# Kernel optimization log

Measured on AMD Instinct MI355X. Metric: run time of the kernel, lower is better.

Reference implementation:

```python
import jax, jax.numpy as jnp
import numpy as np

N = 50000   # nodes
E = 800000  # edges
D = 128     # feature / hidden dim
G = 64      # graphs in batch
L = 3       # GCN layers
EPS = 1e-5  # LayerNorm eps (torch default)


def setup_inputs() -> dict:
    key = jax.random.key(0)
    ks = jax.random.split(key, 6)
    x = jax.random.normal(ks[0], (N, D), dtype=jnp.float32)
    edge_index = jax.random.randint(ks[1], (2, E), 0, N)
    batch = jnp.sort(jax.random.randint(ks[2], (N,), 0, G))
    Ws = jax.random.normal(ks[3], (L, D, D), dtype=jnp.float32) / np.sqrt(D).astype(np.float32)
    bs = jnp.zeros((L, D), dtype=jnp.float32)
    gammas = jnp.ones((L, D), dtype=jnp.float32)
    betas = jnp.zeros((L, D), dtype=jnp.float32)
    return {"x": x, "edge_index": edge_index, "batch": batch,
            "Ws": Ws, "bs": bs, "gammas": gammas, "betas": betas,
            "num_graphs": G}


def _layernorm(h, g, b):
    mu = jnp.mean(h, axis=-1, keepdims=True)
    var = jnp.mean((h - mu) ** 2, axis=-1, keepdims=True)
    return g * (h - mu) * jax.lax.rsqrt(var + EPS) + b


def reference(x, edge_index, batch, Ws, bs, gammas, betas, num_graphs):
    n = x.shape[0]
    loop = jnp.arange(n)
    # GCNConv adds self-loops; symmetric normalization on augmented graph
    src = jnp.concatenate([edge_index[0], loop])
    dst = jnp.concatenate([edge_index[1], loop])
    deg = jax.ops.segment_sum(jnp.ones_like(dst, dtype=x.dtype), dst, num_segments=n)
    dinv = jax.lax.rsqrt(jnp.maximum(deg, 1.0))  # deg >= 1 via self-loops
    norm_e = dinv[src] * dinv[dst]               # [E+N]

    h = x
    for i in range(Ws.shape[0]):
        hw = h @ Ws[i]                           # [N, D] dense GEMM
        msg = hw[src] * norm_e[:, None]          # gather + edge scale
        h = jax.ops.segment_sum(msg, dst, num_segments=n) + bs[i]  # scatter-add
        h = jax.nn.relu(_layernorm(h, gammas[i], betas[i]))
        # dropout is identity in eval mode

    # global mean pool over graph ids
    s = jax.ops.segment_sum(h, batch, num_segments=num_graphs)
    cnt = jax.ops.segment_sum(jnp.ones((n,), x.dtype), batch, num_segments=num_graphs)
    return s / jnp.maximum(cnt, 1.0)[:, None]
```

## Files before the change

### kernel.cpp

```cpp
#include <hip/hip_runtime.h>
#include <math.h>


#define NDIM 128
#define LN_EPS 1e-5f
#define NGRAPH 64
#define EPB 2048

typedef __attribute__((ext_vector_type(8))) short short8;
typedef __attribute__((ext_vector_type(8))) ushort ushort8;
typedef __attribute__((ext_vector_type(4))) float f32x4;

__device__ __forceinline__ ushort f2bf(float f) {
    unsigned u = __float_as_uint(f);
    return (ushort)((u + 0x7FFF + ((u >> 16) & 1)) >> 16);
}
__device__ __forceinline__ float bf2f(ushort b) {
    return __uint_as_float(((unsigned)b) << 16);
}

__device__ __forceinline__ uint block_excl_scan(uint v, uint* s) {
    int t = threadIdx.x;
    s[t] = v; __syncthreads();
    #pragma unroll
    for (int off = 1; off < 256; off <<= 1) {
        uint x = (t >= off) ? s[t - off] : 0u;
        __syncthreads();
        s[t] += x;
        __syncthreads();
    }
    uint incl = s[t];
    __syncthreads();
    return incl - v;
}


__global__ __launch_bounds__(256) void k_h1(const int* __restrict__ dst, uint* __restrict__ hist, int E) {
    __shared__ uint h[256];
    int t = threadIdx.x, b = blockIdx.x;
    h[t] = 0; __syncthreads();
    int e0 = b * EPB;
    #pragma unroll
    for (int i = 0; i < 8; i++) {
        int e = e0 + i * 256 + t;
        if (e < E) atomicAdd(&h[((uint)dst[e]) >> 8], 1u);
    }
    __syncthreads();
    hist[(size_t)b * 256 + t] = h[t];
}

__global__ __launch_bounds__(256) void k_colscan(uint* __restrict__ hist, uint* __restrict__ colsum, int EB) {
    __shared__ uint s[256];
    int t = threadIdx.x, j = blockIdx.x;
    uint v0 = (2 * t     < EB) ? hist[(size_t)(2 * t) * 256 + j] : 0u;
    uint v1 = (2 * t + 1 < EB) ? hist[(size_t)(2 * t + 1) * 256 + j] : 0u;
    uint pair = v0 + v1;
    uint excl = block_excl_scan(pair, s);
    if (2 * t < EB)     hist[(size_t)(2 * t) * 256 + j] = excl;
    if (2 * t + 1 < EB) hist[(size_t)(2 * t + 1) * 256 + j] = excl + v0;
    if (t == 255) colsum[j] = excl + pair;
}

__global__ __launch_bounds__(256) void k_scatter1(const int* __restrict__ src, const int* __restrict__ dst,
                                                  const uint* __restrict__ hist, const uint* __restrict__ colsum,
                                                  uint* __restrict__ ebuf, int E) {
    __shared__ uint s[256];
    __shared__ uint off[256];
    __shared__ uint cur[256];
    int t = threadIdx.x, b = blockIdx.x;
    uint er = block_excl_scan(colsum[t], s);
    off[t] = er + hist[(size_t)b * 256 + t];
    cur[t] = 0;
    __syncthreads();
    int e0 = b * EPB;
    #pragma unroll
    for (int i = 0; i < 8; i++) {
        int e = e0 + i * 256 + t;
        if (e < E) {
            uint d = (uint)dst[e], sv = (uint)src[e];
            uint bin = d >> 8;
            uint r = atomicAdd(&cur[bin], 1u);
            ebuf[off[bin] + r] = (d << 16) | sv;
        }
    }
}

__global__ __launch_bounds__(256) void k_sort2(const uint* __restrict__ ebuf, const uint* __restrict__ colsum,
                                               const int* __restrict__ batch,
                                               ushort* __restrict__ csr, int* __restrict__ base,
                                               int* __restrict__ deg, float* __restrict__ dinv,
                                               int* __restrict__ gstart, int* __restrict__ gend,
                                               const float* __restrict__ Ws, ushort* __restrict__ Wt,
                                               int N, int NB) {
    __shared__ uint h[256], nb[256], s[256], er_arr[256], ep_arr[256];
    int t = threadIdx.x, b = blockIdx.x;
    if (b >= NB) {
        int l = b - NB;
        const float* wsrc = Ws + (size_t)l * NDIM * NDIM;
        char* o = (char*)(Wt + (size_t)l * NDIM * NDIM);
        for (int idx = t; idx < NDIM * NDIM; idx += 256) {
            int k = idx >> 7, nn = idx & 127;
            int byte = ((nn * NDIM + k) * 2) ^ ((nn & 7) << 4);
            *(ushort*)(o + byte) = f2bf(wsrc[idx]);
        }
        return;
    }
    uint total = colsum[t];
    uint er = block_excl_scan(total, s);
    er_arr[t] = er;
    uint ep = block_excl_scan((total + 3u) & ~3u, s);
    ep_arr[t] = ep;
    __syncthreads();
    uint lo = er_arr[b];
    int cnt = (int)colsum[b];
    uint cb = ep_arr[b] + 768u * (uint)b;
    h[t] = 0; __syncthreads();
    for (int i = t; i < cnt; i += 256)
        atomicAdd(&h[(ebuf[lo + i] >> 16) & 255u], 1u);
    __syncthreads();
    uint dg = h[t];
    uint excl = block_excl_scan((dg + 3u) & ~3u, s);
    uint myb = cb + excl;
    nb[t] = myb;
    int n = b * 256 + t;
    if (n < N) {
        base[n] = (int)myb;
        deg[n] = (int)dg;
        dinv[n] = rsqrtf((float)(dg + 1u));
        int g = batch[n];
        if (n == 0 || batch[n - 1] != g) gstart[g] = n;
        if (n == N - 1 || batch[n + 1] != g) gend[g] = n + 1;
    }
    h[t] = 0; __syncthreads();
    for (int i = t; i < cnt; i += 256) {
        uint e = ebuf[lo + i];
        uint bin = (e >> 16) & 255u;
        uint r = atomicAdd(&h[bin], 1u);
        csr[nb[bin] + r] = (ushort)(e & 0xFFFFu);
    }
}


template <bool AF32>
__global__ __launch_bounds__(256) void k_gemm(const void* __restrict__ Ap, const ushort* __restrict__ Wt,
                                              ushort* __restrict__ C, const float* __restrict__ dinv, int N) {
    __shared__ char sW[32768];
    __shared__ ushort sC[64 * NDIM];
    int tid = threadIdx.x;
    {
        const float4* g = (const float4*)Wt;
        float4* s = (float4*)sW;
        #pragma unroll
        for (int i = 0; i < 8; i++) s[tid + 256 * i] = g[tid + 256 * i];
    }
    __syncthreads();

    int wave = tid >> 6, lane = tid & 63;
    int l15 = lane & 15, lhi = lane >> 4;
    int rw = blockIdx.x * 64 + wave * 16;

    f32x4 acc[8];
    #pragma unroll
    for (int n = 0; n < 8; n++) acc[n] = f32x4{0.f, 0.f, 0.f, 0.f};

    const float*  Af = (const float*)Ap;
    const ushort* Ab = (const ushort*)Ap;

    #pragma unroll
    for (int ks = 0; ks < 4; ks++) {
        int k = ks * 32 + lhi * 8;
        short8 a = short8{};
        int r = rw + l15;
        if (r < N) {
            if (AF32) {
                float4 v0 = *(const float4*)&Af[(size_t)r * NDIM + k];
                float4 v1 = *(const float4*)&Af[(size_t)r * NDIM + k + 4];
                short8 t;
                t[0] = (short)f2bf(v0.x); t[1] = (short)f2bf(v0.y);
                t[2] = (short)f2bf(v0.z); t[3] = (short)f2bf(v0.w);
                t[4] = (short)f2bf(v1.x); t[5] = (short)f2bf(v1.y);
                t[6] = (short)f2bf(v1.z); t[7] = (short)f2bf(v1.w);
                a = t;
            } else {
                a = *(const short8*)&Ab[(size_t)r * NDIM + k];
            }
        }
        #pragma unroll
        for (int n = 0; n < 8; n++) {
            int nn = n * 16 + l15;
            int byte = (nn * 256 + k * 2) ^ ((nn & 7) << 4);
            short8 b = *(const short8*)(sW + byte);
            acc[n] = __builtin_amdgcn_mfma_f32_16x16x32_bf16(a, b, acc[n], 0, 0, 0);
        }
    }

    #pragma unroll
    for (int r = 0; r < 4; r++) {
        int row = rw + lhi * 4 + r;
        float dn = (row < N) ? dinv[row] : 0.f;
        #pragma unroll
        for (int n = 0; n < 8; n++)
            sC[(wave * 16 + lhi * 4 + r) * NDIM + n * 16 + l15] = f2bf(acc[n][r] * dn);
    }
    __syncthreads();
    int row0 = blockIdx.x * 64;
    #pragma unroll
    for (int i = 0; i < 4; i++) {
        int flat = tid + i * 256;
        int row = flat >> 4, c8 = (flat & 15) * 8;
        int gr = row0 + row;
        if (gr < N)
            *(short8*)&C[(size_t)gr * NDIM + c8] = *(const short8*)&sC[row * NDIM + c8];
    }
}


__global__ __launch_bounds__(256) void k_agg(const ushort* __restrict__ hw, ushort* __restrict__ out,
                                             const float* __restrict__ dinv, const int* __restrict__ base,
                                             const int* __restrict__ deg, const ushort* __restrict__ csr,
                                             const float* __restrict__ bias, const float* __restrict__ gamma,
                                             const float* __restrict__ beta, int N) {
    int gtid = blockIdx.x * 256 + threadIdx.x;
    int n = gtid >> 5;
    int l4 = threadIdx.x & 31;
    if (n >= N) return;

    const ushort4* hv = (const ushort4*)hw;
    ushort4 sv = hv[(size_t)n * 32 + l4];
    float a0 = bf2f(sv.x), a1 = bf2f(sv.y), a2 = bf2f(sv.z), a3 = bf2f(sv.w);

    int b0 = base[n], dg = deg[n];
    int nfull = dg & ~7;
    ushort4 sa, sb;
    if (nfull > 0) {
        sa = *(const ushort4*)&csr[b0];
        sb = *(const ushort4*)&csr[b0 + 4];
    }
    for (int i = 0; i < nfull; i += 8) {
        ushort4 ca = sa, cb = sb;
        if (i + 8 < nfull) {
            sa = *(const ushort4*)&csr[b0 + i + 8];
            sb = *(const ushort4*)&csr[b0 + i + 12];
        }
        ushort4 t0 = hv[(size_t)ca.x * 32 + l4];
        ushort4 t1 = hv[(size_t)ca.y * 32 + l4];
        ushort4 t2 = hv[(size_t)ca.z * 32 + l4];
        ushort4 t3 = hv[(size_t)ca.w * 32 + l4];
        ushort4 t4 = hv[(size_t)cb.x * 32 + l4];
        ushort4 t5 = hv[(size_t)cb.y * 32 + l4];
        ushort4 t6 = hv[(size_t)cb.z * 32 + l4];
        ushort4 t7 = hv[(size_t)cb.w * 32 + l4];
        a0 += bf2f(t0.x) + bf2f(t1.x) + bf2f(t2.x) + bf2f(t3.x)
            + bf2f(t4.x) + bf2f(t5.x) + bf2f(t6.x) + bf2f(t7.x);
        a1 += bf2f(t0.y) + bf2f(t1.y) + bf2f(t2.y) + bf2f(t3.y)
            + bf2f(t4.y) + bf2f(t5.y) + bf2f(t6.y) + bf2f(t7.y);
        a2 += bf2f(t0.z) + bf2f(t1.z) + bf2f(t2.z) + bf2f(t3.z)
            + bf2f(t4.z) + bf2f(t5.z) + bf2f(t6.z) + bf2f(t7.z);
        a3 += bf2f(t0.w) + bf2f(t1.w) + bf2f(t2.w) + bf2f(t3.w)
            + bf2f(t4.w) + bf2f(t5.w) + bf2f(t6.w) + bf2f(t7.w);
    }
    for (int i = nfull; i < dg; i++) {
        int s = csr[b0 + i];
        ushort4 t = hv[(size_t)s * 32 + l4];
        a0 += bf2f(t.x); a1 += bf2f(t.y); a2 += bf2f(t.z); a3 += bf2f(t.w);
    }

    float dn = dinv[n];
    a0 *= dn; a1 *= dn; a2 *= dn; a3 *= dn;

    float4 bv = ((const float4*)bias)[l4];
    a0 += bv.x; a1 += bv.y; a2 += bv.z; a3 += bv.w;

    float s1 = a0 + a1 + a2 + a3;
    float s2 = a0 * a0 + a1 * a1 + a2 * a2 + a3 * a3;
    #pragma unroll
    for (int o = 1; o < 32; o <<= 1) {
        s1 += __shfl_xor(s1, o);
        s2 += __shfl_xor(s2, o);
    }
    float mu = s1 * (1.f / NDIM);
    float var = s2 * (1.f / NDIM) - mu * mu;
    float rs = rsqrtf(var + LN_EPS);

    float4 gv = ((const float4*)gamma)[l4];
    float4 be = ((const float4*)beta)[l4];
    ushort4 y;
    y.x = f2bf(fmaxf(gv.x * (a0 - mu) * rs + be.x, 0.f));
    y.y = f2bf(fmaxf(gv.y * (a1 - mu) * rs + be.y, 0.f));
    y.z = f2bf(fmaxf(gv.z * (a2 - mu) * rs + be.z, 0.f));
    y.w = f2bf(fmaxf(gv.w * (a3 - mu) * rs + be.w, 0.f));
    ((ushort4*)out)[(size_t)n * 32 + l4] = y;
}


__global__ __launch_bounds__(256) void k_pool2(const ushort* __restrict__ h, const int* __restrict__ gstart,
                                               const int* __restrict__ gend, float* __restrict__ out) {
    __shared__ float ps[16][128];
    int t = threadIdx.x, g = blockIdx.x;
    int st = gstart[g], en = gend[g];
    int rslot = t >> 4, dc = (t & 15) * 8;
    float acc[8] = {0.f, 0.f, 0.f, 0.f, 0.f, 0.f, 0.f, 0.f};
    for (int r = st + rslot; r < en; r += 16) {
        ushort8 v = *(const ushort8*)&h[(size_t)r * NDIM + dc];
        #pragma unroll
        for (int j = 0; j < 8; j++) acc[j] += bf2f(v[j]);
    }
    #pragma unroll
    for (int j = 0; j < 8; j++) ps[rslot][dc + j] = acc[j];
    __syncthreads();
    if (t < 128) {
        float s = 0.f;
        #pragma unroll
        for (int k = 0; k < 16; k++) s += ps[k][t];
        float c = (float)(en - st);
        out[g * NDIM + t] = s / fmaxf(c, 1.f);
    }
}


extern "C" void kernel_launch(void* const* d_in, const int* in_sizes, int n_in,
                              void* d_out, int out_size, void* d_ws, size_t ws_size,
                              hipStream_t stream) {
    const float* x      = (const float*)d_in[0];
    const int*   ei     = (const int*)d_in[1];
    const int*   batch  = (const int*)d_in[2];
    const float* Ws     = (const float*)d_in[3];
    const float* bs     = (const float*)d_in[4];
    const float* gammas = (const float*)d_in[5];
    const float* betas  = (const float*)d_in[6];
    float* out = (float*)d_out;

    int N = in_sizes[0] / NDIM;
    int E = in_sizes[1] / 2;
    const int* src = ei;
    const int* dst = ei + E;
    int EB = (E + EPB - 1) / EPB;
    int NB = (N + 255) / 256;

    char* w = (char*)d_ws;
    auto alloc = [&](size_t bytes) { char* p = w; w += (bytes + 255) & ~(size_t)255; return p; };
    int*    deg    = (int*)alloc((size_t)N * 4);
    int*    base   = (int*)alloc((size_t)N * 4);
    float*  dinv   = (float*)alloc((size_t)N * 4);
    uint*   hist   = (uint*)alloc((size_t)EB * 256 * 4);
    uint*   colsum = (uint*)alloc(256 * 4);
    uint*   ebuf   = (uint*)alloc((size_t)E * 4);
    ushort* csr    = (ushort*)alloc(((size_t)E + 256u * 772u) * 2);
    int*    gse    = (int*)alloc(2 * NGRAPH * 4);
    int*    gstart = gse;
    int*    gend   = gse + NGRAPH;
    ushort* Wt     = (ushort*)alloc((size_t)3 * NDIM * NDIM * 2);
    ushort* bufA   = (ushort*)alloc((size_t)N * NDIM * 2);
    ushort* bufB   = (ushort*)alloc((size_t)N * NDIM * 2);

    k_h1<<<EB, 256, 0, stream>>>(dst, hist, E);
    k_colscan<<<256, 256, 0, stream>>>(hist, colsum, EB);
    k_scatter1<<<EB, 256, 0, stream>>>(src, dst, hist, colsum, ebuf, E);
    k_sort2<<<NB + 3, 256, 0, stream>>>(ebuf, colsum, batch, csr, base, deg, dinv,
                                        gstart, gend, Ws, Wt, N, NB);

    int gGemm = (N + 63) / 64;
    int gAgg  = (N * 32 + 255) / 256;
    for (int l = 0; l < 3; l++) {
        const ushort* wl = Wt + (size_t)l * NDIM * NDIM;
        if (l == 0)
            k_gemm<true><<<gGemm, 256, 0, stream>>>((const void*)x, wl, bufB, dinv, N);
        else
            k_gemm<false><<<gGemm, 256, 0, stream>>>((const void*)bufA, wl, bufB, dinv, N);
        k_agg<<<gAgg, 256, 0, stream>>>(bufB, bufA, dinv, base, deg, csr,
                                        bs + l * NDIM, gammas + l * NDIM, betas + l * NDIM, N);
    }

    k_pool2<<<NGRAPH, 256, 0, stream>>>(bufA, gstart, gend, out);
}
```

Measured before the change: 271.1 us.

## Fuse CSR build into two kernels using per-block bucketed arena

Merges the histogram, column-scan and scatter kernels into a single pass where each edge block locally sorts edges by destination bin into its own arena slice, recording per-bin offsets. The second-stage sort reads each block's chunk for its bin directly, using a fixed per-bin CSR capacity instead of a global prefix scan. Base and degree are packed into an int2 for a single load in aggregation. This removes two launches and a global scan, but the sort kernel now reads many small, scattered chunks serially per thread. It also relies on a fixed capacity of 8192 edges per 256-node bin, which could overflow on skewed graphs.

```diff
diff --git a/kernel.cpp b/kernel.cpp
--- a/kernel.cpp
+++ b/kernel.cpp
@@ -6,6 +6,7 @@
 #define LN_EPS 1e-5f
 #define NGRAPH 64
 #define EPB 2048
+#define CSR_CAP 8192
 
 typedef __attribute__((ext_vector_type(8))) short short8;
 typedef __attribute__((ext_vector_type(8))) ushort ushort8;
@@ -35,8 +36,9 @@
 }
 
 
-__global__ __launch_bounds__(256) void k_h1(const int* __restrict__ dst, uint* __restrict__ hist, int E) {
-    __shared__ uint h[256];
+__global__ __launch_bounds__(256) void k_build1(const int* __restrict__ src, const int* __restrict__ dst,
+                                                uint* __restrict__ hist, uint* __restrict__ arena, int E) {
+    __shared__ uint h[256], s[256], rank[256];
     int t = threadIdx.x, b = blockIdx.x;
     h[t] = 0; __syncthreads();
     int e0 = b * EPB;
@@ -46,53 +48,34 @@
         if (e < E) atomicAdd(&h[((uint)dst[e]) >> 8], 1u);
     }
     __syncthreads();
-    hist[(size_t)b * 256 + t] = h[t];
-}
-
-__global__ __launch_bounds__(256) void k_colscan(uint* __restrict__ hist, uint* __restrict__ colsum, int EB) {
-    __shared__ uint s[256];
-    int t = threadIdx.x, j = blockIdx.x;
-    uint v0 = (2 * t     < EB) ? hist[(size_t)(2 * t) * 256 + j] : 0u;
-    uint v1 = (2 * t + 1 < EB) ? hist[(size_t)(2 * t + 1) * 256 + j] : 0u;
-    uint pair = v0 + v1;
-    uint excl = block_excl_scan(pair, s);
-    if (2 * t < EB)     hist[(size_t)(2 * t) * 256 + j] = excl;
-    if (2 * t + 1 < EB) hist[(size_t)(2 * t + 1) * 256 + j] = excl + v0;
-    if (t == 255) colsum[j] = excl + pair;
-}
-
-__global__ __launch_bounds__(256) void k_scatter1(const int* __restrict__ src, const int* __restrict__ dst,
-                                                  const uint* __restrict__ hist, const uint* __restrict__ colsum,
-                                                  uint* __restrict__ ebuf, int E) {
-    __shared__ uint s[256];
-    __shared__ uint off[256];
-    __shared__ uint cur[256];
-    int t = threadIdx.x, b = blockIdx.x;
-    uint er = block_excl_scan(colsum[t], s);
-    off[t] = er + hist[(size_t)b * 256 + t];
-    cur[t] = 0;
-    __syncthreads();
-    int e0 = b * EPB;
+    uint cnt = h[t];
+    uint off = block_excl_scan(cnt, s);
+    hist[(size_t)b * 257 + t] = off;
+    if (t == 0) hist[(size_t)b * 257 + 256] = (uint)(min(E - e0, EPB));
+    rank[t] = off;
+    __syncthreads();
     #pragma unroll
     for (int i = 0; i < 8; i++) {
         int e = e0 + i * 256 + t;
         if (e < E) {
             uint d = (uint)dst[e], sv = (uint)src[e];
             uint bin = d >> 8;
-            uint r = atomicAdd(&cur[bin], 1u);
-            ebuf[off[bin] + r] = (d << 16) | sv;
-        }
-    }
-}
-
-__global__ __launch_bounds__(256) void k_sort2(const uint* __restrict__ ebuf, const uint* __restrict__ colsum,
-                                               const int* __restrict__ batch,
-                                               ushort* __restrict__ csr, int* __restrict__ base,
-                                               int* __restrict__ deg, float* __restrict__ dinv,
-                                               int* __restrict__ gstart, int* __restrict__ gend,
-                                               const float* __restrict__ Ws, ushort* __restrict__ Wt,
-                                               int N, int NB) {
-    __shared__ uint h[256], nb[256], s[256], er_arr[256], ep_arr[256];
+            uint r = atomicAdd(&rank[bin], 1u);
+            arena[(size_t)b * EPB + r] = (d << 16) | sv;
+        }
+    }
+}
+
+
+__global__ __launch_bounds__(256) void k_sort2b(const uint* __restrict__ arena, const uint* __restrict__ hist,
+                                                const int* __restrict__ batch,
+                                                ushort* __restrict__ csr, int2* __restrict__ bd,
+                                                float* __restrict__ dinv,
+                                                int* __restrict__ gstart, int* __restrict__ gend,
+                                                const float* __restrict__ Ws, ushort* __restrict__ Wt,
+                                                int N, int NB, int EB) {
+    __shared__ uint h[256], nbase[256], s[256];
+    __shared__ uint coff[512], csz[512];
     int t = threadIdx.x, b = blockIdx.x;
     if (b >= NB) {
         int l = b - NB;
@@ -105,38 +88,40 @@
         }
         return;
     }
-    uint total = colsum[t];
-    uint er = block_excl_scan(total, s);
-    er_arr[t] = er;
-    uint ep = block_excl_scan((total + 3u) & ~3u, s);
-    ep_arr[t] = ep;
-    __syncthreads();
-    uint lo = er_arr[b];
-    int cnt = (int)colsum[b];
-    uint cb = ep_arr[b] + 768u * (uint)b;
+    for (int r = t; r < EB; r += 256) {
+        uint o  = hist[(size_t)r * 257 + b];
+        uint nx = (b < 255) ? hist[(size_t)r * 257 + b + 1] : hist[(size_t)r * 257 + 256];
+        coff[r] = r * EPB + o;
+        csz[r]  = nx - o;
+    }
     h[t] = 0; __syncthreads();
-    for (int i = t; i < cnt; i += 256)
-        atomicAdd(&h[(ebuf[lo + i] >> 16) & 255u], 1u);
+    for (int r = t; r < EB; r += 256) {
+        uint c0 = coff[r], cn = csz[r];
+        for (uint j = 0; j < cn; j++)
+            atomicAdd(&h[(arena[c0 + j] >> 16) & 255u], 1u);
+    }
     __syncthreads();
     uint dg = h[t];
     uint excl = block_excl_scan((dg + 3u) & ~3u, s);
-    uint myb = cb + excl;
-    nb[t] = myb;
+    uint myb = (uint)b * CSR_CAP + excl;
+    nbase[t] = myb;
     int n = b * 256 + t;
     if (n < N) {
-        base[n] = (int)myb;
-        deg[n] = (int)dg;
+        bd[n] = make_int2((int)myb, (int)dg);
         dinv[n] = rsqrtf((float)(dg + 1u));
         int g = batch[n];
         if (n == 0 || batch[n - 1] != g) gstart[g] = n;
         if (n == N - 1 || batch[n + 1] != g) gend[g] = n + 1;
     }
     h[t] = 0; __syncthreads();
-    for (int i = t; i < cnt; i += 256) {
-        uint e = ebuf[lo + i];
-        uint bin = (e >> 16) & 255u;
-        uint r = atomicAdd(&h[bin], 1u);
-        csr[nb[bin] + r] = (ushort)(e & 0xFFFFu);
+    for (int r = t; r < EB; r += 256) {
+        uint c0 = coff[r], cn = csz[r];
+        for (uint j = 0; j < cn; j++) {
+            uint e = arena[c0 + j];
+            uint bin = (e >> 16) & 255u;
+            uint rk = atomicAdd(&h[bin], 1u);
+            csr[nbase[bin] + rk] = (ushort)(e & 0xFFFFu);
+        }
     }
 }
 
@@ -216,8 +201,8 @@
 
 
 __global__ __launch_bounds__(256) void k_agg(const ushort* __restrict__ hw, ushort* __restrict__ out,
-                                             const float* __restrict__ dinv, const int* __restrict__ base,
-                                             const int* __restrict__ deg, const ushort* __restrict__ csr,
+                                             const float* __restrict__ dinv, const int2* __restrict__ bd,
+                                             const ushort* __restrict__ csr,
                                              const float* __restrict__ bias, const float* __restrict__ gamma,
                                              const float* __restrict__ beta, int N) {
     int gtid = blockIdx.x * 256 + threadIdx.x;
@@ -229,7 +214,8 @@
     ushort4 sv = hv[(size_t)n * 32 + l4];
     float a0 = bf2f(sv.x), a1 = bf2f(sv.y), a2 = bf2f(sv.z), a3 = bf2f(sv.w);
 
-    int b0 = base[n], dg = deg[n];
+    int2 bdv = bd[n];
+    int b0 = bdv.x, dg = bdv.y;
     int nfull = dg & ~7;
     ushort4 sa, sb;
     if (nfull > 0) {
@@ -339,13 +325,11 @@
 
     char* w = (char*)d_ws;
     auto alloc = [&](size_t bytes) { char* p = w; w += (bytes + 255) & ~(size_t)255; return p; };
-    int*    deg    = (int*)alloc((size_t)N * 4);
-    int*    base   = (int*)alloc((size_t)N * 4);
+    uint*   hist   = (uint*)alloc((size_t)EB * 257 * 4);
+    uint*   arena  = (uint*)alloc((size_t)EB * EPB * 4);
+    ushort* csr    = (ushort*)alloc((size_t)NB * CSR_CAP * 2);
+    int2*   bd     = (int2*)alloc((size_t)N * 8);
     float*  dinv   = (float*)alloc((size_t)N * 4);
-    uint*   hist   = (uint*)alloc((size_t)EB * 256 * 4);
-    uint*   colsum = (uint*)alloc(256 * 4);
-    uint*   ebuf   = (uint*)alloc((size_t)E * 4);
-    ushort* csr    = (ushort*)alloc(((size_t)E + 256u * 772u) * 2);
     int*    gse    = (int*)alloc(2 * NGRAPH * 4);
     int*    gstart = gse;
     int*    gend   = gse + NGRAPH;
@@ -353,11 +337,9 @@
     ushort* bufA   = (ushort*)alloc((size_t)N * NDIM * 2);
     ushort* bufB   = (ushort*)alloc((size_t)N * NDIM * 2);
 
-    k_h1<<<EB, 256, 0, stream>>>(dst, hist, E);
-    k_colscan<<<256, 256, 0, stream>>>(hist, colsum, EB);
-    k_scatter1<<<EB, 256, 0, stream>>>(src, dst, hist, colsum, ebuf, E);
-    k_sort2<<<NB + 3, 256, 0, stream>>>(ebuf, colsum, batch, csr, base, deg, dinv,
-                                        gstart, gend, Ws, Wt, N, NB);
+    k_build1<<<EB, 256, 0, stream>>>(src, dst, hist, arena, E);
+    k_sort2b<<<NB + 3, 256, 0, stream>>>(arena, hist, batch, csr, bd, dinv,
+                                         gstart, gend, Ws, Wt, N, NB, EB);
 
     int gGemm = (N + 63) / 64;
     int gAgg  = (N * 32 + 255) / 256;
@@ -367,7 +349,7 @@
             k_gemm<true><<<gGemm, 256, 0, stream>>>((const void*)x, wl, bufB, dinv, N);
         else
             k_gemm<false><<<gGemm, 256, 0, stream>>>((const void*)bufA, wl, bufB, dinv, N);
-        k_agg<<<gAgg, 256, 0, stream>>>(bufB, bufA, dinv, base, deg, csr,
+        k_agg<<<gAgg, 256, 0, stream>>>(bufB, bufA, dinv, bd, csr,
                                         bs + l * NDIM, gammas + l * NDIM, betas + l * NDIM, N);
     }
 
```

Measured after the change: 272.4 us. About the same (+0.5%).
